# Optimization experiments

Hardware: AMD Instinct MI355X
Metric: run time of the kernel (lower is better)

The kernel has to match this reference:

```python
import jax, jax.numpy as jnp
import numpy as np

B, IN, H = 8192, 512, 2048
DT, TAU_FAST, TAU_SLOW, MEM_TAU = 10.0, 200.0, 1500.0, 100.0
DT_SEC = DT / 1000.0          # 0.01
ALPHA_NEURON = DT / MEM_TAU   # 0.1


def _stsp_buffers(h):
    num_exc = int(np.round(h * 0.8))
    ei = np.ones(h, dtype=np.float32)
    ei[num_exc:] = -1.0
    alpha_stf = np.empty((1, h), np.float32)
    alpha_std = np.empty((1, h), np.float32)
    U = np.empty((1, h), np.float32)
    # exc -> depressing, inh -> facilitating ('exc_dep_inh_fac')
    dep = ei == 1.0
    alpha_stf[0, dep] = DT / TAU_FAST
    alpha_std[0, dep] = DT / TAU_SLOW
    U[0, dep] = 0.45
    alpha_stf[0, ~dep] = DT / TAU_SLOW
    alpha_std[0, ~dep] = DT / TAU_FAST
    U[0, ~dep] = 0.15
    dyn = np.ones((1, h), np.float32)
    mask = (np.ones((h, h)) - np.eye(h)).astype(np.float32)
    return ei, alpha_stf, alpha_std, U, dyn, mask


def setup_inputs() -> dict:
    key = jax.random.key(0)
    ks = jax.random.split(key, 6)
    ei, a_stf, a_std, U, dyn, mask = _stsp_buffers(H)
    rng = np.random.default_rng(0)
    w_ih = np.float32(rng.gamma(0.2, 1.0, size=(IN, H)))
    w_hh = np.float32(rng.gamma(1.0, 1.0, size=(H, H))) * mask
    num_inh = H - int(np.round(H * 0.8))
    return {
        "inp": jax.random.uniform(ks[0], (B, IN), jnp.float32),
        "h_in": jax.random.uniform(ks[1], (B, H), jnp.float32),
        "syn_x": jax.random.uniform(ks[2], (B, H), jnp.float32),
        "syn_u": jax.random.uniform(ks[3], (B, H), jnp.float32),
        "weight_ih": jnp.asarray(w_ih),
        "weight_hh": jnp.asarray(w_hh),
        "bias": jnp.zeros((H,), jnp.float32),
        "alpha_stf": jnp.asarray(a_stf),
        "alpha_std": jnp.asarray(a_std),
        "U": jnp.asarray(U),
        "dynamic_synapse": jnp.asarray(dyn),
        "EI_vec": jnp.asarray(ei),
        "w_mask": jnp.asarray(mask),
    }


def reference(inp, h_in, syn_x, syn_u, weight_ih, weight_hh, bias,
              alpha_stf, alpha_std, U, dynamic_synapse, EI_vec, w_mask):
    # STSP state updates (use pre-update syn_x/syn_u, then clamp)
    syn_x_new = syn_x + (alpha_std * (1.0 - syn_x) - DT_SEC * syn_u * syn_x * h_in) * dynamic_synapse
    syn_u_new = syn_u + (alpha_stf * (U - syn_u) + DT_SEC * U * (1.0 - syn_u) * h_in) * dynamic_synapse
    syn_x_new = jnp.clip(syn_x_new, 0.0, 1.0)
    syn_u_new = jnp.clip(syn_u_new, 0.0, 1.0)
    h_post = syn_u_new * syn_x_new * h_in  # [B, H]
    # EI-constrained recurrent weights: diag(EI) @ relu(W) with zeroed diagonal
    eff_w = w_mask * (EI_vec[:, None] * jax.nn.relu(weight_hh))
    pre = jnp.matmul(inp, jax.nn.relu(weight_ih)) + jnp.matmul(h_post, eff_w) + bias
    h_out = h_in * (1.0 - ALPHA_NEURON) + ALPHA_NEURON * jax.nn.relu(pre)
    return h_out, syn_x_new, syn_u_new
```

## Files before the change

### kernel.cpp

```cpp
#include <hip/hip_runtime.h>
#include <hip/hip_bf16.h>
#include <stdint.h>

#define NB 8192
#define NIN 512
#define NH 2048
#define NK (NIN + NH)
#define NT (NK / 64)

typedef __bf16 bf16;
typedef __bf16 bf16x4 __attribute__((ext_vector_type(4)));
typedef __bf16 bf16x8 __attribute__((ext_vector_type(8)));
typedef float  f32x4  __attribute__((ext_vector_type(4)));

__device__ __forceinline__ void gload16(const void* g, void* l) {
    __builtin_amdgcn_global_load_lds(
        (const __attribute__((address_space(1))) void*)g,
        (__attribute__((address_space(3))) void*)l, 16, 0, 0);
}

#define FENCE()      asm volatile("" ::: "memory")
#define BAR()        do { FENCE(); __builtin_amdgcn_s_barrier(); FENCE(); } while (0)
#define WAIT_LGKM(n) asm volatile("s_waitcnt lgkmcnt(" #n ")" ::: "memory")
#define WAIT_VM(n)   asm volatile("s_waitcnt vmcnt(" #n ")" ::: "memory")

#define EW_BLK ((NB * NH) / (256 * 4))
#define CV_BLK ((NB * NIN) / (256 * 4))
__global__ void ew_kernel(const float* __restrict__ h_in,
                          const float* __restrict__ syn_x,
                          const float* __restrict__ syn_u,
                          const float* __restrict__ a_stf,
                          const float* __restrict__ a_std,
                          const float* __restrict__ Uv,
                          const float* __restrict__ dyn,
                          const float* __restrict__ inp,
                          float* __restrict__ out_sx,
                          float* __restrict__ out_su,
                          bf16* __restrict__ Abuf)
{
    if (blockIdx.x < EW_BLK) {
        int t = blockIdx.x * blockDim.x + threadIdx.x;
        int e = t * 4;
        int row = e >> 11;
        int col = e & 2047;
        f32x4 h    = *(const f32x4*)&h_in[e];
        f32x4 sx   = *(const f32x4*)&syn_x[e];
        f32x4 su   = *(const f32x4*)&syn_u[e];
        f32x4 astf = *(const f32x4*)&a_stf[col];
        f32x4 astd = *(const f32x4*)&a_std[col];
        f32x4 Uq   = *(const f32x4*)&Uv[col];
        f32x4 dq   = *(const f32x4*)&dyn[col];
        f32x4 nsx, nsu;
        bf16x4 hpb;
#pragma unroll
        for (int i = 0; i < 4; ++i) {
            float x = sx[i] + (astd[i] * (1.0f - sx[i]) - 0.01f * su[i] * sx[i] * h[i]) * dq[i];
            float u = su[i] + (astf[i] * (Uq[i] - su[i]) + 0.01f * Uq[i] * (1.0f - su[i]) * h[i]) * dq[i];
            x = fminf(fmaxf(x, 0.0f), 1.0f);
            u = fminf(fmaxf(u, 0.0f), 1.0f);
            nsx[i] = x;
            nsu[i] = u;
            hpb[i] = (bf16)(u * x * h[i]);
        }
        *(f32x4*)&out_sx[e] = nsx;
        *(f32x4*)&out_su[e] = nsu;
        *(bf16x4*)&Abuf[(size_t)row * NK + NIN + col] = hpb;
    } else {
        int t = (blockIdx.x - EW_BLK) * blockDim.x + threadIdx.x;
        int e = t * 4;
        int row = e >> 9;
        int col = e & 511;
        f32x4 v = *(const f32x4*)&inp[e];
        bf16x4 b;
#pragma unroll
        for (int i = 0; i < 4; ++i) b[i] = (bf16)v[i];
        *(bf16x4*)&Abuf[(size_t)row * NK + col] = b;
    }
}

__global__ void prep_w(const float* __restrict__ w_ih,
                       const float* __restrict__ w_hh,
                       const float* __restrict__ w_mask,
                       const float* __restrict__ EI,
                       bf16* __restrict__ Bt)
{
    __shared__ float tile[32][33];
    int b  = blockIdx.x;
    int tk = b % (NK / 32);
    int tn = b / (NK / 32);
    int k0 = tk * 32, n0 = tn * 32;
    int t  = threadIdx.x;
    int lc = t & 31;
    int lr = t >> 5;
#pragma unroll
    for (int it = 0; it < 4; ++it) {
        int kr = lr + it * 8;
        int k  = k0 + kr;
        int n  = n0 + lc;
        float v;
        if (k < NIN) {
            v = fmaxf(w_ih[(size_t)k * NH + n], 0.0f);
        } else {
            int i = k - NIN;
            float w = fmaxf(w_hh[(size_t)i * NH + n], 0.0f);
            v = w_mask[(size_t)i * NH + n] * EI[i] * w;
        }
        tile[kr][lc] = v;
    }
    __syncthreads();
#pragma unroll
    for (int it = 0; it < 4; ++it) {
        int nr = lr + it * 8;
        Bt[(size_t)(n0 + nr) * NK + k0 + lc] = (bf16)tile[lc][nr];
    }
}

__global__ __launch_bounds__(512, 2)
void gemm_fused(const bf16* __restrict__ A,
                const bf16* __restrict__ Bt,
                const float* __restrict__ h_in,
                const float* __restrict__ bias,
                float* __restrict__ h_out)
{
    __shared__ bf16 sA[2][16384];
    __shared__ bf16 sB[2][16384];

    const int bid  = blockIdx.x;
    const int bid2 = (bid & 7) * 32 + (bid >> 3);
    const int tm = bid2 >> 3, tn = bid2 & 7;
    const int rowBase = tm * 256, colBase = tn * 256;

    const int tid  = threadIdx.x;
    const int wid  = tid >> 6, lane = tid & 63;
    const int wr   = wid >> 2, wc = wid & 3;
    const int ln15 = lane & 15, l4 = lane >> 4;

    const int sr  = lane >> 3;
    const int gcs = (((lane & 7) ^ sr) << 3);
    const int sk0 = ((l4 ^ (ln15 & 7)) << 3);
    const int sk1 = sk0 ^ 32;

    f32x4 acc[8][4];
#pragma unroll
    for (int i = 0; i < 8; ++i)
#pragma unroll
        for (int j = 0; j < 4; ++j) acc[i][j] = (f32x4){0.f, 0.f, 0.f, 0.f};

    bf16x8 af[4][2], bf0[2][2], bf1[2][2];

    auto stA = [&](bf16* dst, int T, int u) {
#pragma unroll
        for (int w = 0; w < 2; ++w) {
            int gr = rowBase + w * 128 + u * 64 + wid * 8 + sr;
            gload16(A + (size_t)gr * NK + T * 64 + gcs,
                    dst + u * 8192 + w * 4096 + wid * 512);
        }
    };
    auto stB = [&](bf16* dst, int T, int u) {
#pragma unroll
        for (int w = 0; w < 2; ++w) {
            int gn = colBase + (w * 2 + (wid >> 2)) * 64 + u * 32 + (wid & 3) * 8 + sr;
            gload16(Bt + (size_t)gn * NK + T * 64 + gcs,
                    dst + u * 8192 + w * 4096 + wid * 512);
        }
    };

#define READ_A(MH) do {                                                        \
    const bf16* _ba = &sAc[(MH) * 8192 + wr * 4096 + ln15 * 64];               \
    _Pragma("unroll") for (int m = 0; m < 4; ++m) {                            \
        af[m][0] = *(const bf16x8*)(_ba + m * 1024 + sk0);                     \
        af[m][1] = *(const bf16x8*)(_ba + m * 1024 + sk1); } } while (0)

#define READ_B(NHALF, bfr) do {                                                \
    const bf16* _bb = &sBc[(NHALF) * 8192 + wc * 2048 + ln15 * 64];            \
    _Pragma("unroll") for (int n = 0; n < 2; ++n) {                            \
        bfr[n][0] = *(const bf16x8*)(_bb + n * 1024 + sk0);                    \
        bfr[n][1] = *(const bf16x8*)(_bb + n * 1024 + sk1); } } while (0)

#define MFMAQ(MH, NHALF, bfr) do {                                             \
    _Pragma("unroll") for (int kk = 0; kk < 2; ++kk)                           \
    _Pragma("unroll") for (int m = 0; m < 4; ++m)                              \
    _Pragma("unroll") for (int n = 0; n < 2; ++n)                              \
        acc[(MH) * 4 + m][(NHALF) * 2 + n] =                                   \
            __builtin_amdgcn_mfma_f32_16x16x32_bf16(                           \
                af[m][kk], bfr[n][kk],                                         \
                acc[(MH) * 4 + m][(NHALF) * 2 + n], 0, 0, 0);                  \
    } while (0)

#define TILE(t, sAc_, sBc_, sAn_, sBn_, S1, S2, VMW) do {                      \
    const bf16* sAc = sAc_; const bf16* sBc = sBc_;                            \
    READ_A(0); READ_B(0, bf0); FENCE();                                        \
    READ_B(1, bf1); FENCE();                                                   \
    if (S1) stA(sAn_, (t) + 1, 1);                                             \
    WAIT_LGKM(4);                                              \
    __builtin_amdgcn_s_setprio(1);                                             \
    MFMAQ(0, 0, bf0);                                                          \
    WAIT_LGKM(0);                                                 \
    MFMAQ(0, 1, bf1);                                                          \
    __builtin_amdgcn_s_setprio(0);                                             \
    READ_A(1); FENCE();                                                        \
    BAR();                 \
    if (S2) { stA((bf16*)sAc_, (t) + 2, 0);                                    \
              stB((bf16*)sBc_, (t) + 2, 0);                                    \
              stB((bf16*)sBc_, (t) + 2, 1); }                                  \
    __builtin_amdgcn_s_setprio(1);                                             \
    MFMAQ(1, 1, bf1);                                                          \
    MFMAQ(1, 0, bf0);                                                          \
    __builtin_amdgcn_s_setprio(0);                                             \
    VMW;                                                                       \
    BAR(); } while (0)

    stA(sA[0], 0, 0); stB(sB[0], 0, 0); stB(sB[0], 0, 1); stA(sA[0], 0, 1);
    stA(sA[1], 1, 0); stB(sB[1], 1, 0); stB(sB[1], 1, 1);
    WAIT_VM(6);
    BAR();

    for (int t = 0; t < NT - 2; t += 2) {
        TILE(t,     sA[0], sB[0], sA[1], sB[1], 1, 1, WAIT_VM(6));
        TILE(t + 1, sA[1], sB[1], sA[0], sB[0], 1, 1, WAIT_VM(6));
    }
    TILE(NT - 2, sA[0], sB[0], sA[1], sB[1], 1, 0, WAIT_VM(0));
    TILE(NT - 1, sA[1], sB[1], sA[0], sB[0], 0, 0, FENCE());

#pragma unroll
    for (int mf = 0; mf < 8; ++mf) {
#pragma unroll
        for (int nf = 0; nf < 4; ++nf) {
            int col = colBase + wc * 64 + nf * 16 + ln15;
            float bv = bias[col];
            int row0 = rowBase + wr * 128 + mf * 16 + l4 * 4;
#pragma unroll
            for (int r = 0; r < 4; ++r) {
                size_t idx = (size_t)(row0 + r) * NH + col;
                float pre = acc[mf][nf][r] + bv;
                h_out[idx] = 0.9f * h_in[idx] + 0.1f * fmaxf(pre, 0.0f);
            }
        }
    }
#undef READ_A
#undef READ_B
#undef MFMAQ
#undef TILE
}

extern "C" void kernel_launch(void* const* d_in, const int* in_sizes, int n_in,
                              void* d_out, int out_size, void* d_ws, size_t ws_size,
                              hipStream_t stream)
{
    const float* inp    = (const float*)d_in[0];
    const float* h_in   = (const float*)d_in[1];
    const float* syn_x  = (const float*)d_in[2];
    const float* syn_u  = (const float*)d_in[3];
    const float* w_ih   = (const float*)d_in[4];
    const float* w_hh   = (const float*)d_in[5];
    const float* bias   = (const float*)d_in[6];
    const float* a_stf  = (const float*)d_in[7];
    const float* a_std  = (const float*)d_in[8];
    const float* Uv     = (const float*)d_in[9];
    const float* dyn    = (const float*)d_in[10];
    const float* EI     = (const float*)d_in[11];
    const float* w_mask = (const float*)d_in[12];

    float* out   = (float*)d_out;
    float* out_h = out;
    float* out_x = out + (size_t)NB * NH;
    float* out_u = out + 2 * (size_t)NB * NH;

    bf16* Abuf = (bf16*)d_ws;
    bf16* Btw  = Abuf + (size_t)NB * NK;

    ew_kernel<<<EW_BLK + CV_BLK, 256, 0, stream>>>(
        h_in, syn_x, syn_u, a_stf, a_std, Uv, dyn, inp, out_x, out_u, Abuf);
    prep_w<<<(NK / 32) * (NH / 32), 256, 0, stream>>>(w_ih, w_hh, w_mask, EI, Btw);
    gemm_fused<<<(NB / 256) * (NH / 256), 512, 0, stream>>>(Abuf, Btw, h_in, bias, out_h);
}
```

Before: 174.1 us.

## Split A-fragment LDS reads into halves and grid-stride the elementwise kernel

The GEMM inner tile now loads A fragments in two 2-row halves (afA/afB) and interleaves them with MFMA groups and finer lgkmcnt waits. This cuts register pressure and overlaps LDS reads with matrix math instead of loading all four A fragments up front. The elementwise/convert kernel becomes a grid-stride loop over a fixed 2048-block grid instead of one block per 1024 elements, which reduces block launch overhead. The cost is more wait points and scheduling complexity in the hot loop, and the fixed grid may give less memory-level parallelism.

```diff
diff --git a/kernel.cpp b/kernel.cpp
--- a/kernel.cpp
+++ b/kernel.cpp
@@ -24,8 +24,10 @@
 #define WAIT_LGKM(n) asm volatile("s_waitcnt lgkmcnt(" #n ")" ::: "memory")
 #define WAIT_VM(n)   asm volatile("s_waitcnt vmcnt(" #n ")" ::: "memory")
 
-#define EW_BLK ((NB * NH) / (256 * 4))
-#define CV_BLK ((NB * NIN) / (256 * 4))
+#define EW_ITEMS ((NB * NH) / 4)
+#define CV_ITEMS ((NB * NIN) / 4)
+#define TOT_ITEMS (EW_ITEMS + CV_ITEMS)
+#define EW_GRID  2048
 __global__ void ew_kernel(const float* __restrict__ h_in,
                           const float* __restrict__ syn_x,
                           const float* __restrict__ syn_u,
@@ -38,43 +40,44 @@
                           float* __restrict__ out_su,
                           bf16* __restrict__ Abuf)
 {
-    if (blockIdx.x < EW_BLK) {
-        int t = blockIdx.x * blockDim.x + threadIdx.x;
-        int e = t * 4;
-        int row = e >> 11;
-        int col = e & 2047;
-        f32x4 h    = *(const f32x4*)&h_in[e];
-        f32x4 sx   = *(const f32x4*)&syn_x[e];
-        f32x4 su   = *(const f32x4*)&syn_u[e];
-        f32x4 astf = *(const f32x4*)&a_stf[col];
-        f32x4 astd = *(const f32x4*)&a_std[col];
-        f32x4 Uq   = *(const f32x4*)&Uv[col];
-        f32x4 dq   = *(const f32x4*)&dyn[col];
-        f32x4 nsx, nsu;
-        bf16x4 hpb;
-#pragma unroll
-        for (int i = 0; i < 4; ++i) {
-            float x = sx[i] + (astd[i] * (1.0f - sx[i]) - 0.01f * su[i] * sx[i] * h[i]) * dq[i];
-            float u = su[i] + (astf[i] * (Uq[i] - su[i]) + 0.01f * Uq[i] * (1.0f - su[i]) * h[i]) * dq[i];
-            x = fminf(fmaxf(x, 0.0f), 1.0f);
-            u = fminf(fmaxf(u, 0.0f), 1.0f);
-            nsx[i] = x;
-            nsu[i] = u;
-            hpb[i] = (bf16)(u * x * h[i]);
-        }
-        *(f32x4*)&out_sx[e] = nsx;
-        *(f32x4*)&out_su[e] = nsu;
-        *(bf16x4*)&Abuf[(size_t)row * NK + NIN + col] = hpb;
-    } else {
-        int t = (blockIdx.x - EW_BLK) * blockDim.x + threadIdx.x;
-        int e = t * 4;
-        int row = e >> 9;
-        int col = e & 511;
-        f32x4 v = *(const f32x4*)&inp[e];
-        bf16x4 b;
-#pragma unroll
-        for (int i = 0; i < 4; ++i) b[i] = (bf16)v[i];
-        *(bf16x4*)&Abuf[(size_t)row * NK + col] = b;
+    const int stride = EW_GRID * 256;
+    for (int i = blockIdx.x * 256 + threadIdx.x; i < TOT_ITEMS; i += stride) {
+        if (i < EW_ITEMS) {
+            int e = i * 4;
+            int row = e >> 11;
+            int col = e & 2047;
+            f32x4 h    = *(const f32x4*)&h_in[e];
+            f32x4 sx   = *(const f32x4*)&syn_x[e];
+            f32x4 su   = *(const f32x4*)&syn_u[e];
+            f32x4 astf = *(const f32x4*)&a_stf[col];
+            f32x4 astd = *(const f32x4*)&a_std[col];
+            f32x4 Uq   = *(const f32x4*)&Uv[col];
+            f32x4 dq   = *(const f32x4*)&dyn[col];
+            f32x4 nsx, nsu;
+            bf16x4 hpb;
+#pragma unroll
+            for (int k = 0; k < 4; ++k) {
+                float x = sx[k] + (astd[k] * (1.0f - sx[k]) - 0.01f * su[k] * sx[k] * h[k]) * dq[k];
+                float u = su[k] + (astf[k] * (Uq[k] - su[k]) + 0.01f * Uq[k] * (1.0f - su[k]) * h[k]) * dq[k];
+                x = fminf(fmaxf(x, 0.0f), 1.0f);
+                u = fminf(fmaxf(u, 0.0f), 1.0f);
+                nsx[k] = x;
+                nsu[k] = u;
+                hpb[k] = (bf16)(u * x * h[k]);
+            }
+            *(f32x4*)&out_sx[e] = nsx;
+            *(f32x4*)&out_su[e] = nsu;
+            *(bf16x4*)&Abuf[(size_t)row * NK + NIN + col] = hpb;
+        } else {
+            int e = (i - EW_ITEMS) * 4;
+            int row = e >> 9;
+            int col = e & 511;
+            f32x4 v = *(const f32x4*)&inp[e];
+            bf16x4 b;
+#pragma unroll
+            for (int k = 0; k < 4; ++k) b[k] = (bf16)v[k];
+            *(bf16x4*)&Abuf[(size_t)row * NK + col] = b;
+        }
     }
 }
 
@@ -146,7 +149,7 @@
 #pragma unroll
         for (int j = 0; j < 4; ++j) acc[i][j] = (f32x4){0.f, 0.f, 0.f, 0.f};
 
-    bf16x8 af[4][2], bf0[2][2], bf1[2][2];
+    bf16x8 afA[2][2], afB[2][2], bf0[2][2], bf1[2][2];
 
     auto stA = [&](bf16* dst, int T, int u) {
 #pragma unroll
@@ -165,47 +168,61 @@
         }
     };
 
-#define READ_A(MH) do {                                                        \
-    const bf16* _ba = &sAc[(MH) * 8192 + wr * 4096 + ln15 * 64];               \
-    _Pragma("unroll") for (int m = 0; m < 4; ++m) {                            \
-        af[m][0] = *(const bf16x8*)(_ba + m * 1024 + sk0);                     \
-        af[m][1] = *(const bf16x8*)(_ba + m * 1024 + sk1); } } while (0)
-
-#define READ_B(NHALF, bfr) do {                                                \
+#define READ_A2(dst, MH, MP) do {                                              \
+    const bf16* _ba = &sAc[(MH) * 8192 + wr * 4096 + (MP) * 2048 + ln15 * 64]; \
+    _Pragma("unroll") for (int mi = 0; mi < 2; ++mi) {                         \
+        dst[mi][0] = *(const bf16x8*)(_ba + mi * 1024 + sk0);                  \
+        dst[mi][1] = *(const bf16x8*)(_ba + mi * 1024 + sk1); } } while (0)
+
+#define READ_B4(NHALF, bfr) do {                                               \
     const bf16* _bb = &sBc[(NHALF) * 8192 + wc * 2048 + ln15 * 64];            \
     _Pragma("unroll") for (int n = 0; n < 2; ++n) {                            \
         bfr[n][0] = *(const bf16x8*)(_bb + n * 1024 + sk0);                    \
         bfr[n][1] = *(const bf16x8*)(_bb + n * 1024 + sk1); } } while (0)
 
-#define MFMAQ(MH, NHALF, bfr) do {                                             \
+#define MFMA8(afp, MH, MP, NHALF, bfr) do {                                    \
     _Pragma("unroll") for (int kk = 0; kk < 2; ++kk)                           \
-    _Pragma("unroll") for (int m = 0; m < 4; ++m)                              \
+    _Pragma("unroll") for (int mi = 0; mi < 2; ++mi)                           \
     _Pragma("unroll") for (int n = 0; n < 2; ++n)                              \
-        acc[(MH) * 4 + m][(NHALF) * 2 + n] =                                   \
+        acc[(MH) * 4 + (MP) * 2 + mi][(NHALF) * 2 + n] =                       \
             __builtin_amdgcn_mfma_f32_16x16x32_bf16(                           \
-                af[m][kk], bfr[n][kk],                                         \
-                acc[(MH) * 4 + m][(NHALF) * 2 + n], 0, 0, 0);                  \
+                afp[mi][kk], bfr[n][kk],                                       \
+                acc[(MH) * 4 + (MP) * 2 + mi][(NHALF) * 2 + n], 0, 0, 0);      \
     } while (0)
 
 #define TILE(t, sAc_, sBc_, sAn_, sBn_, S1, S2, VMW) do {                      \
     const bf16* sAc = sAc_; const bf16* sBc = sBc_;                            \
-    READ_A(0); READ_B(0, bf0); FENCE();                                        \
-    READ_B(1, bf1); FENCE();                                                   \
+    READ_A2(afA, 0, 0); FENCE();                                       \
+    READ_B4(0, bf0);    FENCE();                                       \
+    READ_A2(afB, 0, 1); FENCE();                                       \
+    READ_B4(1, bf1);    FENCE();                                       \
     if (S1) stA(sAn_, (t) + 1, 1);                                             \
-    WAIT_LGKM(4);                                              \
-    __builtin_amdgcn_s_setprio(1);                                             \
-    MFMAQ(0, 0, bf0);                                                          \
-    WAIT_LGKM(0);                                                 \
-    MFMAQ(0, 1, bf1);                                                          \
-    __builtin_amdgcn_s_setprio(0);                                             \
-    READ_A(1); FENCE();                                                        \
-    BAR();                 \
+    WAIT_LGKM(8);                                            \
+    __builtin_amdgcn_s_setprio(1);                                             \
+    MFMA8(afA, 0, 0, 0, bf0);                                                  \
+    WAIT_LGKM(4);                                                \
+    MFMA8(afB, 0, 1, 0, bf0);                                                  \
+    WAIT_LGKM(0);                                                \
+    MFMA8(afA, 0, 0, 1, bf1);                                                  \
+    __builtin_amdgcn_s_setprio(0);                                             \
+    READ_A2(afA, 1, 0); FENCE();        \
+    __builtin_amdgcn_s_setprio(1);                                             \
+    MFMA8(afB, 0, 1, 1, bf1);                                                  \
+    __builtin_amdgcn_s_setprio(0);                                             \
+    READ_A2(afB, 1, 1); FENCE();                           \
+    __builtin_amdgcn_s_setprio(1);                                             \
+    WAIT_LGKM(4);                                            \
+    MFMA8(afA, 1, 0, 1, bf1);                                                  \
+    WAIT_LGKM(0);                                            \
+    MFMA8(afB, 1, 1, 1, bf1);                                                  \
+    __builtin_amdgcn_s_setprio(0);                                             \
+    BAR();            \
     if (S2) { stA((bf16*)sAc_, (t) + 2, 0);                                    \
               stB((bf16*)sBc_, (t) + 2, 0);                                    \
               stB((bf16*)sBc_, (t) + 2, 1); }                                  \
     __builtin_amdgcn_s_setprio(1);                                             \
-    MFMAQ(1, 1, bf1);                                                          \
-    MFMAQ(1, 0, bf0);                                                          \
+    MFMA8(afA, 1, 0, 0, bf0);                                                  \
+    MFMA8(afB, 1, 1, 0, bf0);                                                  \
     __builtin_amdgcn_s_setprio(0);                                             \
     VMW;                                                                       \
     BAR(); } while (0)
@@ -237,9 +254,9 @@
             }
         }
     }
-#undef READ_A
-#undef READ_B
-#undef MFMAQ
+#undef READ_A2
+#undef READ_B4
+#undef MFMA8
 #undef TILE
 }
 
@@ -269,7 +286,7 @@
     bf16* Abuf = (bf16*)d_ws;
     bf16* Btw  = Abuf + (size_t)NB * NK;
 
-    ew_kernel<<<EW_BLK + CV_BLK, 256, 0, stream>>>(
+    ew_kernel<<<EW_GRID, 256, 0, stream>>>(
         h_in, syn_x, syn_u, a_stf, a_std, Uv, dyn, inp, out_x, out_u, Abuf);
     prep_w<<<(NK / 32) * (NH / 32), 256, 0, stream>>>(w_ih, w_hh, w_mask, EI, Btw);
     gemm_fused<<<(NB / 256) * (NH / 256), 512, 0, stream>>>(Abuf, Btw, h_in, bias, out_h);
```

After: 184.7 us. +6.1%, slower.
